# Kernel tuning notes

Hardware: AMD Instinct MI355X
Metric: run time of the kernel (lower is better)

The kernel has to match this reference:

```python
import jax, jax.numpy as jnp
import numpy as np

B, D, N, H = 2, 8, 40, 128
HID = 4 * H  # 512, MLP hidden width


def setup_inputs() -> dict:
    key = jax.random.key(0)
    ks = jax.random.split(key, 12)
    s_in = 1.0 / np.sqrt(2 * H)
    s_hid = 1.0 / np.sqrt(HID)
    return {
        "node_feature": jax.random.normal(ks[0], (B, D, N, H), jnp.float32),
        "pairwise_feature": jax.random.normal(ks[1], (B, D, N, N, H), jnp.float32),
        # first MLP layer weight [2H, HID] split into node half and pairwise half
        "W1n": jax.random.uniform(ks[2], (H, HID), jnp.float32, -s_in, s_in),
        "W1p": jax.random.uniform(ks[3], (H, HID), jnp.float32, -s_in, s_in),
        "b1": jax.random.uniform(ks[4], (HID,), jnp.float32, -s_in, s_in),
        "W2": jax.random.uniform(ks[5], (HID, HID), jnp.float32, -s_hid, s_hid),
        "b2": jax.random.uniform(ks[6], (HID,), jnp.float32, -s_hid, s_hid),
        "W3": jax.random.uniform(ks[7], (HID, 1), jnp.float32, -s_hid, s_hid),
        "b3": jax.random.uniform(ks[8], (1,), jnp.float32, -s_hid, s_hid),
        "scale": jnp.float32(1.0),
        "bias": jnp.float32(0.0),
    }


def reference(node_feature, pairwise_feature, W1n, W1p, b1, W2, b2, W3, b3, scale, bias):
    # max over the dataset axis
    nf = jnp.max(node_feature, axis=-3)        # [B, N, H]
    pf = jnp.max(pairwise_feature, axis=-4)    # [B, N, N, H]
    # First linear on concat([node_expand, pair_expand]) decomposed into two
    # small projections + broadcast add (mathematically identical to
    # Linear(concat) since W1 = [W1n; W1p]).
    hn = nf @ W1n                               # [B, N, HID]
    hp = pf @ W1p                               # [B, N, N, HID]
    h = jax.nn.relu(hn[:, :, None, None, :] + hp[:, None, :, :, :] + b1)  # [B,N,N,N,HID]
    h = jax.nn.relu(h @ W2 + b2)                # [B, N, N, N, HID]
    v = h @ W3 + b3                             # [B, N, N, N, 1]
    return jax.nn.sigmoid(scale * v + bias).squeeze(-1)  # [B, N, N, N]
```

## Files before the change

### kernel.cpp

```cpp
#include <hip/hip_runtime.h>
#include <math.h>

#define BB 2
#define DD 8
#define NN 40
#define HH 128
#define HID 512
#define NJK 1600
#define MROW 64000

typedef __attribute__((ext_vector_type(8))) short short8;
typedef __attribute__((ext_vector_type(4))) float floatx4;

static __device__ __forceinline__ unsigned short f2bf(float x) {
    unsigned int b = __float_as_uint(x);
    b += 0x7fffu + ((b >> 16) & 1u);
    return (unsigned short)(b >> 16);
}

__global__ __launch_bounds__(256) void prep_kernel(
        const float* __restrict__ node, const float* __restrict__ pair,
        const float* __restrict__ W1n, const float* __restrict__ W1p,
        const float* __restrict__ b1, const float* __restrict__ W2,
        float* __restrict__ hp, float* __restrict__ hnb,
        unsigned short* __restrict__ w2f) {
    __shared__ float smem[32 * 513];
    const int bid = blockIdx.x;
    const int t = threadIdx.x;

    if (bid < 400) {
        float (*pf)[HH] = (float (*)[HH])smem;
        const int rowbase = bid * 8;
        #pragma unroll
        for (int e = t; e < 8*HH; e += 256) {
            int r8 = e >> 7, c = e & 127;
            int grow = rowbase + r8;
            int b = grow / NJK, jk = grow - b*NJK;
            float m = -INFINITY;
            #pragma unroll
            for (int d = 0; d < DD; ++d)
                m = fmaxf(m, pair[((size_t)((b*DD + d)*NJK + jk))*HH + c]);
            pf[r8][c] = m;
        }
        __syncthreads();
        const int rg = t >> 7, c4 = (t & 127) * 4;
        float4 acc[4];
        #pragma unroll
        for (int r = 0; r < 4; ++r) acc[r] = make_float4(0.f,0.f,0.f,0.f);
        #pragma unroll 4
        for (int h = 0; h < HH; ++h) {
            float4 wv = *(const float4*)&W1p[h*HID + c4];
            #pragma unroll
            for (int r = 0; r < 4; ++r) {
                float pv = pf[rg*4 + r][h];
                acc[r].x = fmaf(pv, wv.x, acc[r].x);
                acc[r].y = fmaf(pv, wv.y, acc[r].y);
                acc[r].z = fmaf(pv, wv.z, acc[r].z);
                acc[r].w = fmaf(pv, wv.w, acc[r].w);
            }
        }
        #pragma unroll
        for (int r = 0; r < 4; ++r)
            *(float4*)&hp[(size_t)(rowbase + rg*4 + r)*HID + c4] = acc[r];
    } else if (bid < 410) {
        float (*nf)[HH] = (float (*)[HH])smem;
        const int rowbase = (bid - 400) * 8;
        #pragma unroll
        for (int e = t; e < 8*HH; e += 256) {
            int r8 = e >> 7, c = e & 127;
            int grow = rowbase + r8;
            int b = grow / NN, i = grow - b*NN;
            float m = -INFINITY;
            #pragma unroll
            for (int d = 0; d < DD; ++d)
                m = fmaxf(m, node[((size_t)((b*DD + d)*NN + i))*HH + c]);
            nf[r8][c] = m;
        }
        __syncthreads();
        const int rg = t >> 7, c4 = (t & 127) * 4;
        float4 acc[4];
        #pragma unroll
        for (int r = 0; r < 4; ++r) acc[r] = make_float4(0.f,0.f,0.f,0.f);
        #pragma unroll 4
        for (int h = 0; h < HH; ++h) {
            float4 wv = *(const float4*)&W1n[h*HID + c4];
            #pragma unroll
            for (int r = 0; r < 4; ++r) {
                float nv = nf[rg*4 + r][h];
                acc[r].x = fmaf(nv, wv.x, acc[r].x);
                acc[r].y = fmaf(nv, wv.y, acc[r].y);
                acc[r].z = fmaf(nv, wv.z, acc[r].z);
                acc[r].w = fmaf(nv, wv.w, acc[r].w);
            }
        }
        float4 b1v = *(const float4*)&b1[c4];
        #pragma unroll
        for (int r = 0; r < 4; ++r) {
            float4 o = make_float4(acc[r].x + b1v.x, acc[r].y + b1v.y,
                                   acc[r].z + b1v.z, acc[r].w + b1v.w);
            *(float4*)&hnb[(size_t)(rowbase + rg*4 + r)*HID + c4] = o;
        }
    } else {
        const int ks = bid - 410;
        for (int e = t; e < 32*HID; e += 256) {
            int r = e >> 9, c = e & 511;
            smem[r*513 + c] = W2[(size_t)(ks*32 + r)*HID + c];
        }
        __syncthreads();
        const int w = t >> 6, l = t & 63;
        const int lr = l & 15, lg = l >> 4;
        #pragma unroll
        for (int f = 0; f < 8; ++f) {
            int cf = w*8 + f;
            short8 u;
            #pragma unroll
            for (int kk = 0; kk < 8; ++kk)
                u[kk] = (short)f2bf(smem[(lg*8 + kk)*513 + cf*16 + lr]);
            *(short8*)(w2f + (size_t)(cf*16 + ks)*512 + l*8) = u;
        }
    }
}

__global__ __launch_bounds__(512, 2) void main_kernel(
        const float* __restrict__ hp, const float* __restrict__ hnb,
        const unsigned short* __restrict__ w2f,
        const float* __restrict__ b2, const float* __restrict__ W3,
        const float* __restrict__ b3, const float* __restrict__ scale,
        const float* __restrict__ bias, float* __restrict__ out) {
    __shared__ unsigned short h1s[128 * HID];
    __shared__ float red[8][128];

    const int bid  = blockIdx.x;
    const int bid8 = (bid & 7)*125 + (bid >> 3);
    const int b    = bid8 / 500;
    const int rr_  = bid8 % 500;
    const int i0   = (rr_ / 100) * 8;
    const int jk0  = (rr_ % 100) * 16;
    const int t    = threadIdx.x;
    char* h1c = (char*)h1s;

    const float* hpb  = hp  + ((size_t)b*NJK + jk0)*HID;
    const float* hnbb = hnb + ((size_t)(b*NN + i0))*HID;
    #pragma unroll 4
    for (int it = 0; it < 16; ++it) {
        int g   = it*512 + t;
        int row = g >> 6, k8 = g & 63;
        int il  = row >> 4, jl = row & 15;
        const float* hr = hpb  + (size_t)jl*HID + k8*8;
        const float* nr = hnbb + (size_t)il*HID + k8*8;
        float4 p0 = *(const float4*)hr, p1 = *(const float4*)(hr + 4);
        float4 n0 = *(const float4*)nr, n1 = *(const float4*)(nr + 4);
        short8 u;
        u[0] = (short)f2bf(fmaxf(p0.x + n0.x, 0.f));
        u[1] = (short)f2bf(fmaxf(p0.y + n0.y, 0.f));
        u[2] = (short)f2bf(fmaxf(p0.z + n0.z, 0.f));
        u[3] = (short)f2bf(fmaxf(p0.w + n0.w, 0.f));
        u[4] = (short)f2bf(fmaxf(p1.x + n1.x, 0.f));
        u[5] = (short)f2bf(fmaxf(p1.y + n1.y, 0.f));
        u[6] = (short)f2bf(fmaxf(p1.z + n1.z, 0.f));
        u[7] = (short)f2bf(fmaxf(p1.w + n1.w, 0.f));
        int off = ((row << 10) + (k8 << 4)) ^ ((row & 7) << 4);
        *(short8*)(h1c + off) = u;
    }
    __syncthreads();

    const int w  = t >> 6, l = t & 63;
    const int lr = l & 15, lg = l >> 4;
    const int swz = (lr & 7) << 4;

    floatx4 acc[8][4];
    #pragma unroll
    for (int mi = 0; mi < 8; ++mi)
        #pragma unroll
        for (int tn = 0; tn < 4; ++tn)
            acc[mi][tn] = (floatx4){0.f, 0.f, 0.f, 0.f};

    const unsigned short* bbase = w2f + (size_t)w*32768 + l*8;

    short8 bcur[4];
    #pragma unroll
    for (int tn = 0; tn < 4; ++tn)
        bcur[tn] = *(const short8*)(bbase + ((tn*16 + 0) << 9));

    #pragma unroll 1
    for (int ks = 0; ks < 16; ++ks) {
        short8 bnxt[4];
        int ksn = (ks + 1) & 15;
        #pragma unroll
        for (int tn = 0; tn < 4; ++tn)
            bnxt[tn] = *(const short8*)(bbase + ((tn*16 + ksn) << 9));
        short8 av[8];
        #pragma unroll
        for (int mi = 0; mi < 8; ++mi) {
            int aoff = (((mi*16 + lr) << 10) + (ks << 6) + (lg << 4)) ^ swz;
            av[mi] = *(const short8*)(h1c + aoff);
        }
        #pragma unroll
        for (int mi = 0; mi < 8; ++mi)
            #pragma unroll
            for (int tn = 0; tn < 4; ++tn)
                acc[mi][tn] = __builtin_amdgcn_mfma_f32_16x16x32_bf16(av[mi], bcur[tn], acc[mi][tn], 0, 0, 0);
        #pragma unroll
        for (int tn = 0; tn < 4; ++tn) bcur[tn] = bnxt[tn];
    }

    float b2v[4], w3v[4];
    #pragma unroll
    for (int tn = 0; tn < 4; ++tn) {
        int col = w*64 + tn*16 + lr;
        b2v[tn] = b2[col];
        w3v[tn] = W3[col];
    }
    #pragma unroll
    for (int mi = 0; mi < 8; ++mi) {
        #pragma unroll
        for (int q = 0; q < 4; ++q) {
            float s = 0.f;
            #pragma unroll
            for (int tn = 0; tn < 4; ++tn)
                s += fmaxf(acc[mi][tn][q] + b2v[tn], 0.f) * w3v[tn];
            s += __shfl_xor(s, 1);
            s += __shfl_xor(s, 2);
            s += __shfl_xor(s, 4);
            s += __shfl_xor(s, 8);
            if (lr == 0) red[w][mi*16 + lg*4 + q] = s;
        }
    }
    __syncthreads();
    if (t < 128) {
        float v = b3[0];
        #pragma unroll
        for (int c = 0; c < 8; ++c) v += red[c][t];
        float z = scale[0]*v + bias[0];
        int il = t >> 4, jl = t & 15;
        out[(size_t)b*MROW + (size_t)(i0 + il)*NJK + jk0 + jl] =
            1.0f / (1.0f + expf(-z));
    }
}

extern "C" void kernel_launch(void* const* d_in, const int* in_sizes, int n_in,
                              void* d_out, int out_size, void* d_ws, size_t ws_size,
                              hipStream_t stream) {
    const float* node  = (const float*)d_in[0];
    const float* pair  = (const float*)d_in[1];
    const float* W1n   = (const float*)d_in[2];
    const float* W1p   = (const float*)d_in[3];
    const float* b1    = (const float*)d_in[4];
    const float* W2    = (const float*)d_in[5];
    const float* b2    = (const float*)d_in[6];
    const float* W3    = (const float*)d_in[7];
    const float* b3    = (const float*)d_in[8];
    const float* scale = (const float*)d_in[9];
    const float* bias  = (const float*)d_in[10];
    float* out = (float*)d_out;

    float* hp = (float*)d_ws;
    float* hnb = hp + (size_t)BB*NJK*HID;
    unsigned short* w2f = (unsigned short*)(hnb + BB*NN*HID);

    hipLaunchKernelGGL(prep_kernel, dim3(426), dim3(256), 0, stream,
                       node, pair, W1n, W1p, b1, W2, hp, hnb, w2f);
    hipLaunchKernelGGL(main_kernel, dim3(1000), dim3(512), 0, stream,
                       hp, hnb, w2f, b2, W3, b3, scale, bias, out);
}
```

Before: 179.5 us.

## Materialize bf16 first-layer activations in global memory and stream via global_load_lds

Adds a prep pass that builds the relu(hp+hn) first-layer activations as bf16 in an MFMA-fragment layout in workspace (about 131 MB). A new GEMM kernel then streams these tiles straight into LDS with a triple-buffered global_load_lds pipeline and prefetches the W2 fragments from global memory. This removes the per-block on-the-fly construction of the 128x512 activation tile in LDS, at the cost of a large extra HBM write and read. The old path is kept as a fallback when the workspace is too small.

```diff
diff --git a/kernel.cpp b/kernel.cpp
--- a/kernel.cpp
+++ b/kernel.cpp
@@ -16,6 +16,12 @@
     unsigned int b = __float_as_uint(x);
     b += 0x7fffu + ((b >> 16) & 1u);
     return (unsigned short)(b >> 16);
+}
+
+static __device__ __forceinline__ void gload_lds16(const void* g, void* l) {
+    __builtin_amdgcn_global_load_lds(
+        (const __attribute__((address_space(1))) unsigned int*)g,
+        (__attribute__((address_space(3))) unsigned int*)l, 16, 0, 0);
 }
 
 __global__ __launch_bounds__(256) void prep_kernel(
@@ -118,6 +124,132 @@
                 u[kk] = (short)f2bf(smem[(lg*8 + kk)*513 + cf*16 + lr]);
             *(short8*)(w2f + (size_t)(cf*16 + ks)*512 + l*8) = u;
         }
+    }
+}
+
+__global__ __launch_bounds__(256) void prep2_kernel(
+        const float* __restrict__ hp, const float* __restrict__ hnb,
+        unsigned short* __restrict__ h1f) {
+    const int p = blockIdx.x;
+    const int t = threadIdx.x;
+    #pragma unroll 4
+    for (int j = 0; j < 32; ++j) {
+        int s  = j*256 + t;
+        int ks = s >> 9, mi = (s >> 6) & 7, l = s & 63;
+        int grow = p*128 + mi*16 + (l & 15);
+        int b  = grow / MROW;
+        int r  = grow - b*MROW;
+        int i  = r / NJK;
+        int jk = r - i*NJK;
+        int k0 = ks*32 + (l >> 4)*8;
+        const float* hr = hp  + ((size_t)b*NJK + jk)*HID + k0;
+        const float* nr = hnb + ((size_t)(b*NN + i))*HID + k0;
+        float4 p0 = *(const float4*)hr, p1 = *(const float4*)(hr + 4);
+        float4 n0 = *(const float4*)nr, n1 = *(const float4*)(nr + 4);
+        short8 u;
+        u[0] = (short)f2bf(fmaxf(p0.x + n0.x, 0.f));
+        u[1] = (short)f2bf(fmaxf(p0.y + n0.y, 0.f));
+        u[2] = (short)f2bf(fmaxf(p0.z + n0.z, 0.f));
+        u[3] = (short)f2bf(fmaxf(p0.w + n0.w, 0.f));
+        u[4] = (short)f2bf(fmaxf(p1.x + n1.x, 0.f));
+        u[5] = (short)f2bf(fmaxf(p1.y + n1.y, 0.f));
+        u[6] = (short)f2bf(fmaxf(p1.z + n1.z, 0.f));
+        u[7] = (short)f2bf(fmaxf(p1.w + n1.w, 0.f));
+        *(short8*)(h1f + (size_t)p*65536 + (size_t)s*8) = u;
+    }
+}
+
+__global__ __launch_bounds__(512, 2) void main2_kernel(
+        const unsigned short* __restrict__ h1f,
+        const unsigned short* __restrict__ w2f,
+        const float* __restrict__ b2, const float* __restrict__ W3,
+        const float* __restrict__ b3, const float* __restrict__ scale,
+        const float* __restrict__ bias, float* __restrict__ out) {
+    __shared__ __align__(16) unsigned short asl[3 * 4096];
+    __shared__ float red[8][128];
+
+    const int p = blockIdx.x;
+    const int t = threadIdx.x;
+    const int w = t >> 6, l = t & 63;
+    const int lr = l & 15, lg = l >> 4;
+
+    const unsigned short* ablk = h1f + (size_t)p*65536;
+    #define ISSUE_A(ks, buf) \
+        gload_lds16(ablk + (ks)*4096 + w*512 + l*8, &asl[(buf)*4096 + w*512])
+
+    floatx4 acc[8][4];
+    #pragma unroll
+    for (int mi = 0; mi < 8; ++mi)
+        #pragma unroll
+        for (int tn = 0; tn < 4; ++tn)
+            acc[mi][tn] = (floatx4){0.f, 0.f, 0.f, 0.f};
+
+    const unsigned short* bbase = w2f + (size_t)w*32768 + l*8;
+
+    ISSUE_A(0, 0);
+    ISSUE_A(1, 1);
+    short8 bcur[4];
+    #pragma unroll
+    for (int tn = 0; tn < 4; ++tn)
+        bcur[tn] = *(const short8*)(bbase + ((tn*16) << 9));
+
+    #pragma unroll 1
+    for (int ks = 0; ks < 16; ++ks) {
+        __builtin_amdgcn_s_barrier();
+        if (ks < 14) {
+            int buf = (ks + 2) % 3;
+            ISSUE_A(ks + 2, buf);
+        }
+        short8 bnxt[4];
+        int ksn = (ks + 1) & 15;
+        #pragma unroll
+        for (int tn = 0; tn < 4; ++tn)
+            bnxt[tn] = *(const short8*)(bbase + ((tn*16 + ksn) << 9));
+        asm volatile("s_waitcnt vmcnt(5)" ::: "memory");
+        __builtin_amdgcn_sched_barrier(0);
+
+        const unsigned short* sl = asl + (ks % 3) * 4096;
+        #pragma unroll
+        for (int mi = 0; mi < 8; ++mi) {
+            short8 a = *(const short8*)(sl + mi*512 + l*8);
+            #pragma unroll
+            for (int tn = 0; tn < 4; ++tn)
+                acc[mi][tn] = __builtin_amdgcn_mfma_f32_16x16x32_bf16(a, bcur[tn], acc[mi][tn], 0, 0, 0);
+        }
+        #pragma unroll
+        for (int tn = 0; tn < 4; ++tn) bcur[tn] = bnxt[tn];
+    }
+    #undef ISSUE_A
+
+    float b2v[4], w3v[4];
+    #pragma unroll
+    for (int tn = 0; tn < 4; ++tn) {
+        int col = w*64 + tn*16 + lr;
+        b2v[tn] = b2[col];
+        w3v[tn] = W3[col];
+    }
+    #pragma unroll
+    for (int mi = 0; mi < 8; ++mi) {
+        #pragma unroll
+        for (int q = 0; q < 4; ++q) {
+            float s = 0.f;
+            #pragma unroll
+            for (int tn = 0; tn < 4; ++tn)
+                s += fmaxf(acc[mi][tn][q] + b2v[tn], 0.f) * w3v[tn];
+            s += __shfl_xor(s, 1);
+            s += __shfl_xor(s, 2);
+            s += __shfl_xor(s, 4);
+            s += __shfl_xor(s, 8);
+            if (lr == 0) red[w][mi*16 + lg*4 + q] = s;
+        }
+    }
+    __syncthreads();
+    if (t < 128) {
+        float v = b3[0];
+        #pragma unroll
+        for (int c = 0; c < 8; ++c) v += red[c][t];
+        float z = scale[0]*v + bias[0];
+        out[(size_t)p*128 + t] = 1.0f / (1.0f + expf(-z));
     }
 }
 
@@ -254,12 +386,22 @@
     const float* bias  = (const float*)d_in[10];
     float* out = (float*)d_out;
 
-    float* hp = (float*)d_ws;
+    float* hp  = (float*)d_ws;
     float* hnb = hp + (size_t)BB*NJK*HID;
     unsigned short* w2f = (unsigned short*)(hnb + BB*NN*HID);
+    unsigned short* h1f = w2f + 262144;
+
+    const size_t need = 6553600ull + 163840ull + 524288ull + 131072000ull;
 
     hipLaunchKernelGGL(prep_kernel, dim3(426), dim3(256), 0, stream,
                        node, pair, W1n, W1p, b1, W2, hp, hnb, w2f);
-    hipLaunchKernelGGL(main_kernel, dim3(1000), dim3(512), 0, stream,
-                       hp, hnb, w2f, b2, W3, b3, scale, bias, out);
-}
+    if (ws_size >= need) {
+        hipLaunchKernelGGL(prep2_kernel, dim3(1000), dim3(256), 0, stream,
+                           hp, hnb, h1f);
+        hipLaunchKernelGGL(main2_kernel, dim3(1000), dim3(512), 0, stream,
+                           h1f, w2f, b2, W3, b3, scale, bias, out);
+    } else {
+        hipLaunchKernelGGL(main_kernel, dim3(1000), dim3(512), 0, stream,
+                           hp, hnb, w2f, b2, W3, b3, scale, bias, out);
+    }
+}
```

After: 232.7 us. 1.3x slower.
